# Kernel optimization log

Hardware: AMD Instinct MI355X
Metric: run time of the kernel (lower is better)

Reference implementation:

```python
import jax, jax.numpy as jnp
import numpy as np

B, Q, K, D, H, DH = 4, 512, 4096, 1024, 8, 128  # qk_channels=v_channels=out=1024

def setup_inputs() -> dict:
    key = jax.random.key(0)
    ks = jax.random.split(key, 5)
    s = 1.0 / np.sqrt(D)
    return {
        "inputs_q": jax.random.normal(ks[0], (B, Q, D), jnp.float32),
        "inputs_kv": jax.random.normal(ks[1], (B, K, D), jnp.float32),
        "Wq": jax.random.normal(ks[2], (D, H, DH), jnp.float32) * s,
        "Wkv": jax.random.normal(ks[3], (D, H, 2 * DH), jnp.float32) * s,
        "Wproj": jax.random.normal(ks[4], (H, DH, D), jnp.float32) * (1.0 / np.sqrt(H * DH)),
        "b_proj": jnp.zeros((D,), jnp.float32),
    }

def reference(inputs_q, inputs_kv, Wq, Wkv, Wproj, b_proj):
    # QKV projections (no bias)
    q = jnp.einsum('bqd,dhe->bqhe', inputs_q, Wq)          # [B,Q,H,DH]
    kv = jnp.einsum('bkd,dhe->bkhe', inputs_kv, Wkv)        # [B,K,H,2*DH]
    k, v = kv[..., :DH], kv[..., DH:]
    # scaled dot-product attention (softmax in fp32, per source)
    attn = jnp.einsum('bqhd,bkhd->bhqk', q, k) / np.sqrt(DH)
    attn = jax.nn.softmax(attn.astype(jnp.float32), axis=-1).astype(v.dtype)
    o = jnp.einsum('bhqk,bkhd->bqhd', attn, v)              # [B,Q,H,DH]
    # output projection contracting (head, head_dim), with bias
    return jnp.einsum('bqhd,hdo->bqo', o, Wproj) + b_proj   # [B,Q,D]
```

## Files before the change

kernel.cpp:

```cpp
#include <hip/hip_runtime.h>
#include <hip/hip_bf16.h>
#include <cstdint>

typedef unsigned short u16;
typedef unsigned int u32;
typedef __bf16 bf16x8 __attribute__((ext_vector_type(8)));
typedef u16 u16x8 __attribute__((ext_vector_type(8)));
typedef u16 u16x4 __attribute__((ext_vector_type(4)));
typedef float f32x4 __attribute__((ext_vector_type(4)));

#define MFMA16(a, b, c) __builtin_amdgcn_mfma_f32_16x16x32_bf16(a, b, c, 0, 0, 0)

__device__ __forceinline__ void async16(const void* g, void* s) {
    __builtin_amdgcn_global_load_lds((const __attribute__((address_space(1))) void*)g,
                                     (__attribute__((address_space(3))) void*)s, 16, 0, 0);
}

__device__ __forceinline__ u16 f2bf(float f) {
    u32 u; __builtin_memcpy(&u, &f, 4);
    u = u + 0x7fffu + ((u >> 16) & 1u);
    return (u16)(u >> 16);
}

__global__ __launch_bounds__(256) void convert_inputs(const float* __restrict__ inq,
                                                      u16* __restrict__ Aq,
                                                      const float* __restrict__ inkv,
                                                      u16* __restrict__ Akv) {
    const int blk = blockIdx.x;
    const float* in; u16* out; size_t i;
    if (blk < 1024) { in = inq;  out = Aq;  i = (size_t)blk * 256 + threadIdx.x; }
    else            { in = inkv; out = Akv; i = (size_t)(blk - 1024) * 256 + threadIdx.x; }
    const float4* p = (const float4*)in + i * 2;
    const float4 a = p[0], b = p[1];
    u16x8 v;
    v[0] = f2bf(a.x); v[1] = f2bf(a.y); v[2] = f2bf(a.z); v[3] = f2bf(a.w);
    v[4] = f2bf(b.x); v[5] = f2bf(b.y); v[6] = f2bf(b.z); v[7] = f2bf(b.w);
    ((u16x8*)out)[i] = v;
}

__global__ __launch_bounds__(256) void prep_weights(const float* __restrict__ Wq,  u16* __restrict__ WqT,
                                                    const float* __restrict__ Wkv, u16* __restrict__ WkvT,
                                                    const float* __restrict__ Wp,  u16* __restrict__ WpT) {
    __shared__ u16 t[64][65];
    const int blk = blockIdx.x;
    const float* in; u16* out; int R, C, bx, by;
    if (blk < 256)      { in = Wq;  out = WqT;  R = 1024; C = 1024; bx = blk & 15;  by = blk >> 4; }
    else if (blk < 768) { in = Wkv; out = WkvT; R = 1024; C = 2048; bx = (blk - 256) & 31; by = (blk - 256) >> 5; }
    else                { in = Wp;  out = WpT;  R = 1024; C = 1024; bx = (blk - 768) & 15; by = (blk - 768) >> 4; }
    const int r0 = by << 6, c0 = bx << 6;
    const int tid = threadIdx.x;
#pragma unroll
    for (int i = 0; i < 16; i++) {
        int idx = i * 256 + tid;
        int r = idx >> 6, c = idx & 63;
        t[r][c] = f2bf(in[(size_t)(r0 + r) * C + c0 + c]);
    }
    __syncthreads();
#pragma unroll
    for (int i = 0; i < 16; i++) {
        int idx = i * 256 + tid;
        int c = idx >> 6, r = idx & 63;
        out[(size_t)(c0 + c) * R + r0 + r] = t[r][c];
    }
}

template <bool OUTF32, int NT>
__global__ __launch_bounds__(256) void gemm_bt(const u16* __restrict__ A,
                                               const u16* __restrict__ B,
                                               void* __restrict__ Cv,
                                               const float* __restrict__ bias,
                                               int M, int N, int K) {
    constexpr int NJ = NT / 32;
    __shared__ __align__(16) u16 As[128 * 64];
    __shared__ __align__(16) u16 Bs[NT * 64];
    const int tid = threadIdx.x;
    const int wave = tid >> 6, lane = tid & 63;
    const int lrow = lane & 15, quad = lane >> 4;
    const int nb = N / NT;
    const int bx = blockIdx.x % nb, by = blockIdx.x / nb;
    const long m0 = (long)by << 7, n0 = (long)bx * NT;
    const int wm = (wave >> 1) << 6, wn = (wave & 1) * (NT / 2);

    const f32x4 fz = {0.f, 0.f, 0.f, 0.f};
    f32x4 acc[4][NJ];
#pragma unroll
    for (int i = 0; i < 4; i++)
#pragma unroll
        for (int j = 0; j < NJ; j++) acc[i][j] = fz;

    const int srow = wave * 8 + (lane >> 3);
    const int scol = ((lane & 7) ^ (lane >> 3)) << 3;
    const u16* Ag = A + (m0 + srow) * K + scol;
    const u16* Bg = B + (n0 + srow) * K + scol;
    u16* AsW = &As[wave * 512];
    u16* BsW = &Bs[wave * 512];

    for (int k0 = 0; k0 < K; k0 += 64) {
        __syncthreads();
#pragma unroll
        for (int c = 0; c < 4; c++)
            async16(Ag + (long)c * 32 * K + k0, AsW + c * 2048);
#pragma unroll
        for (int c = 0; c < NT / 32; c++)
            async16(Bg + (long)c * 32 * K + k0, BsW + c * 2048);
        __syncthreads();
#pragma unroll
        for (int c = 0; c < 2; c++) {
            bf16x8 af[4], bfr[NJ];
#pragma unroll
            for (int i = 0; i < 4; i++) {
                const int row = wm + i * 16 + lrow;
                af[i] = *(const bf16x8*)&As[row * 64 + (((c * 4 + quad) ^ (row & 7)) << 3)];
            }
#pragma unroll
            for (int j = 0; j < NJ; j++) {
                const int row = wn + j * 16 + lrow;
                bfr[j] = *(const bf16x8*)&Bs[row * 64 + (((c * 4 + quad) ^ (row & 7)) << 3)];
            }
#pragma unroll
            for (int i = 0; i < 4; i++)
#pragma unroll
                for (int j = 0; j < NJ; j++)
                    acc[i][j] = MFMA16(af[i], bfr[j], acc[i][j]);
        }
    }
#pragma unroll
    for (int j = 0; j < NJ; j++) {
        const long col = n0 + wn + j * 16 + lrow;
        const float bv = bias ? bias[col] : 0.0f;
#pragma unroll
        for (int i = 0; i < 4; i++) {
            const long row = m0 + wm + i * 16 + quad * 4;
#pragma unroll
            for (int r = 0; r < 4; r++) {
                const float v = acc[i][j][r] + bv;
                if (OUTF32) ((float*)Cv)[(row + r) * N + col] = v;
                else        ((u16*)Cv)[(row + r) * N + col] = f2bf(v);
            }
        }
    }
}

__global__ __launch_bounds__(512, 2) void gemm_kv256(const u16* __restrict__ A,
                                                     const u16* __restrict__ B,
                                                     u16* __restrict__ C,
                                                     u16* __restrict__ Vt) {
    constexpr int K = 1024, N = 2048, NT = 16;
    __shared__ __align__(16) u16 As[2][256 * 64];
    __shared__ __align__(16) u16 Bs[2][256 * 64];
    const int tid = threadIdx.x;
    const int wave = tid >> 6, lane = tid & 63;
    const int lrow = lane & 15, quad = lane >> 4;
    const int wMi = wave >> 2, wNi = wave & 3;
    const int wm = wMi * 128, wn = wNi * 64;
    const int wg = blockIdx.x;
    const int swz = (wg & 7) * 64 + (wg >> 3);
    const int bx = swz & 7, by = swz >> 3;
    const long m0 = (long)by << 8, n0 = (long)bx << 8;

    const int srow = tid >> 3;
    const int scol = ((tid & 7) ^ (srow & 7)) << 3;
    const u16* Ag = A + (m0 + srow) * K + scol;
    const u16* Bg = B + (n0 + srow) * K + scol;
    const int sdst = tid * 8;

    auto stgA = [&](int bi, int h, int kt) {
        async16(Ag + (size_t)(h * 128) * K + kt * 64,      &As[bi][h * 8192 + sdst]);
        async16(Ag + (size_t)(h * 128 + 64) * K + kt * 64, &As[bi][h * 8192 + 4096 + sdst]);
    };
    auto stgB = [&](int bi, int h, int kt) {
        async16(Bg + (size_t)(h * 128) * K + kt * 64,      &Bs[bi][h * 8192 + sdst]);
        async16(Bg + (size_t)(h * 128 + 64) * K + kt * 64, &Bs[bi][h * 8192 + 4096 + sdst]);
    };

    stgB(0, 0, 0); stgB(0, 1, 0); stgA(0, 0, 0); stgA(0, 1, 0);
    stgB(1, 0, 1); stgB(1, 1, 1); stgA(1, 0, 1);

    const f32x4 fz = {0.f, 0.f, 0.f, 0.f};
    f32x4 acc[8][4];
#pragma unroll
    for (int i = 0; i < 8; i++)
#pragma unroll
        for (int j = 0; j < 4; j++) acc[i][j] = fz;

    asm volatile("s_waitcnt vmcnt(6)" ::: "memory");
    __builtin_amdgcn_s_barrier();

    bf16x8 av[4][2], bv[4][2];
    for (int t = 0; t < NT; ++t) {
        const int cur = t & 1, nxt = cur ^ 1;
#pragma unroll
        for (int i = 0; i < 4; i++) {
            const int row = wm + i * 16 + lrow;
#pragma unroll
            for (int c = 0; c < 2; c++)
                av[i][c] = *(const bf16x8*)&As[cur][row * 64 + (((c * 4 + quad) ^ (row & 7)) << 3)];
        }
#pragma unroll
        for (int j = 0; j < 4; j++) {
            const int row = wn + j * 16 + lrow;
#pragma unroll
            for (int c = 0; c < 2; c++)
                bv[j][c] = *(const bf16x8*)&Bs[cur][row * 64 + (((c * 4 + quad) ^ (row & 7)) << 3)];
        }
        if (t + 1 < NT) stgA(nxt, 1, t + 1);
        __builtin_amdgcn_s_barrier();
        asm volatile("s_waitcnt lgkmcnt(0)" ::: "memory");
        __builtin_amdgcn_s_setprio(1);
#pragma unroll
        for (int i = 0; i < 4; i++)
#pragma unroll
            for (int j = 0; j < 2; j++)
#pragma unroll
                for (int c = 0; c < 2; c++)
                    acc[i][j] = MFMA16(av[i][c], bv[j][c], acc[i][j]);
        __builtin_amdgcn_s_setprio(0);
        __builtin_amdgcn_s_barrier();
        if (t + 2 < NT) stgB(cur, 0, t + 2);
        __builtin_amdgcn_s_barrier();
        __builtin_amdgcn_s_setprio(1);
#pragma unroll
        for (int i = 0; i < 4; i++)
#pragma unroll
            for (int j = 2; j < 4; j++)
#pragma unroll
                for (int c = 0; c < 2; c++)
                    acc[i][j] = MFMA16(av[i][c], bv[j][c], acc[i][j]);
        __builtin_amdgcn_s_setprio(0);
        __builtin_amdgcn_s_barrier();
#pragma unroll
        for (int i = 0; i < 4; i++) {
            const int row = wm + (i + 4) * 16 + lrow;
#pragma unroll
            for (int c = 0; c < 2; c++)
                av[i][c] = *(const bf16x8*)&As[cur][row * 64 + (((c * 4 + quad) ^ (row & 7)) << 3)];
        }
        if (t + 2 < NT) stgB(cur, 1, t + 2);
        __builtin_amdgcn_s_barrier();
        asm volatile("s_waitcnt lgkmcnt(0)" ::: "memory");
        __builtin_amdgcn_s_setprio(1);
#pragma unroll
        for (int i = 0; i < 4; i++)
#pragma unroll
            for (int j = 0; j < 2; j++)
#pragma unroll
                for (int c = 0; c < 2; c++)
                    acc[i + 4][j] = MFMA16(av[i][c], bv[j][c], acc[i + 4][j]);
        __builtin_amdgcn_s_setprio(0);
        __builtin_amdgcn_s_barrier();
        if (t + 2 < NT) stgA(cur, 0, t + 2);
        __builtin_amdgcn_s_barrier();
        __builtin_amdgcn_s_setprio(1);
#pragma unroll
        for (int i = 0; i < 4; i++)
#pragma unroll
            for (int j = 2; j < 4; j++)
#pragma unroll
                for (int c = 0; c < 2; c++)
                    acc[i + 4][j] = MFMA16(av[i][c], bv[j][c], acc[i + 4][j]);
        __builtin_amdgcn_s_setprio(0);
        if (t + 2 < NT)      { asm volatile("s_waitcnt vmcnt(6)" ::: "memory"); }
        else if (t + 1 < NT) { asm volatile("s_waitcnt vmcnt(0)" ::: "memory"); }
        __builtin_amdgcn_s_barrier();
    }

    const int h = bx;
    if (wNi < 2) {
#pragma unroll
        for (int j = 0; j < 4; j++) {
            const long col = n0 + wn + j * 16 + lrow;
#pragma unroll
            for (int i = 0; i < 8; i++) {
                const long row = m0 + wm + i * 16 + quad * 4;
#pragma unroll
                for (int r = 0; r < 4; r++)
                    C[(row + r) * N + col] = f2bf(acc[i][j][r]);
            }
        }
    } else {
#pragma unroll
        for (int j = 0; j < 4; j++) {
            const int dh = (wNi - 2) * 64 + j * 16 + lrow;
#pragma unroll
            for (int i = 0; i < 8; i++) {
                const int row = (int)m0 + wm + i * 16 + quad * 4;
                const int b = row >> 12, kv = row & 4095;
                u16x4 pk;
#pragma unroll
                for (int r = 0; r < 4; r++) pk[r] = f2bf(acc[i][j][r]);
                *(u16x4*)&Vt[(((size_t)b * 8 + h) * 128 + dh) * 4096 + kv] = pk;
            }
        }
    }
}

__global__ __launch_bounds__(512) void flash_attn_split(const u16* __restrict__ qb,
                                                        const u16* __restrict__ kvb,
                                                        const u16* __restrict__ vTb,
                                                        float* __restrict__ Opart,
                                                        float* __restrict__ Mpart,
                                                        float* __restrict__ Lpart) {
    __shared__ __align__(16) u16 Ks[64 * 128];
    __shared__ __align__(16) u16 Vs[128 * 64];
    __shared__ __align__(16) u16 Ps[8][16 * 64];
    const int tid = threadIdx.x, wave = tid >> 6, lane = tid & 63;
    const int lrow = lane & 15, quad = lane >> 4;
    const int blk = blockIdx.x;
    const int split = blk & 3, qt = (blk >> 2) & 3, h = (blk >> 4) & 7, b = blk >> 7;
    const int q0 = qt * 128;
    const int kbase = split * 1024;

    bf16x8 qf[4];
    {
        const u16* qp = qb + (((size_t)(b * 512 + q0 + wave * 16 + lrow) * 8 + h) << 7) + quad * 8;
#pragma unroll
        for (int c = 0; c < 4; c++) qf[c] = *(const bf16x8*)(qp + c * 32);
    }

    const f32x4 fz = {0.f, 0.f, 0.f, 0.f};
    f32x4 oacc[8];
#pragma unroll
    for (int g = 0; g < 8; g++) oacc[g] = fz;
    float mrow = -1e30f, lsum = 0.f;
    const float scale = 0.08838834764831845f;

    const int kRow = tid >> 4, kBlk = tid & 15;
    const int vRow = tid >> 3, vBlk = tid & 7;
    const u16* kg = kvb + (size_t)b * 4096 * 2048 + h * 256 + kBlk * 8;
    const u16* vg = vTb + (size_t)(b * 8 + h) * 128 * 4096 + vBlk * 8;

    for (int k0 = kbase; k0 < kbase + 1024; k0 += 64) {
        __syncthreads();
#pragma unroll
        for (int i = 0; i < 2; i++) {
            const int r = i * 32 + kRow;
            *(bf16x8*)&Ks[r * 128 + ((kBlk ^ (r & 15)) << 3)] =
                *(const bf16x8*)&kg[(size_t)(k0 + r) * 2048];
            const int rv = i * 64 + vRow;
            *(bf16x8*)&Vs[rv * 64 + ((vBlk ^ (rv & 7)) << 3)] =
                *(const bf16x8*)&vg[(size_t)rv * 4096 + k0];
        }
        __syncthreads();

        f32x4 s[4];
#pragma unroll
        for (int t = 0; t < 4; t++) {
            f32x4 a = fz;
#pragma unroll
            for (int c = 0; c < 4; c++) {
                const bf16x8 kf = *(const bf16x8*)
                    &Ks[(t * 16 + lrow) * 128 + (((c * 4 + quad) ^ lrow) << 3)];
                a = MFMA16(kf, qf[c], a);
            }
            s[t] = a * scale;
        }

        float mx = s[0][0];
#pragma unroll
        for (int t = 0; t < 4; t++)
#pragma unroll
            for (int r = 0; r < 4; r++) mx = fmaxf(mx, s[t][r]);
        mx = fmaxf(mx, __shfl_xor(mx, 16));
        mx = fmaxf(mx, __shfl_xor(mx, 32));
        const float mn = fmaxf(mrow, mx);
        const float alpha = __expf(mrow - mn);
        mrow = mn;
        float sum = 0.f;
#pragma unroll
        for (int t = 0; t < 4; t++)
#pragma unroll
            for (int r = 0; r < 4; r++) {
                float p = __expf(s[t][r] - mn);
                s[t][r] = p;
                sum += p;
            }
        sum += __shfl_xor(sum, 16);
        sum += __shfl_xor(sum, 32);
        lsum = lsum * alpha + sum;

        u16* Pw = &Ps[wave][0];
#pragma unroll
        for (int t = 0; t < 4; t++) {
            u16x4 pk;
#pragma unroll
            for (int r = 0; r < 4; r++) pk[r] = f2bf(s[t][r]);
            const int kvo = t * 16 + quad * 4;
            *(u16x4*)&Pw[lrow * 64 + (((kvo >> 3) ^ (lrow & 7)) << 3) + (kvo & 7)] = pk;
        }
        asm volatile("s_waitcnt lgkmcnt(0)" ::: "memory");
        const bf16x8 pf0 = *(const bf16x8*)&Pw[lrow * 64 + ((quad ^ (lrow & 7)) << 3)];
        const bf16x8 pf1 = *(const bf16x8*)&Pw[lrow * 64 + (((4 + quad) ^ (lrow & 7)) << 3)];

#pragma unroll
        for (int g = 0; g < 8; g++) {
            f32x4 o = oacc[g] * alpha;
            o = MFMA16(*(const bf16x8*)&Vs[(g * 16 + lrow) * 64 + ((quad ^ (lrow & 7)) << 3)], pf0, o);
            o = MFMA16(*(const bf16x8*)&Vs[(g * 16 + lrow) * 64 + (((4 + quad) ^ (lrow & 7)) << 3)], pf1, o);
            oacc[g] = o;
        }
    }

    float* Ob = Opart + (size_t)blk * 16384;
#pragma unroll
    for (int g = 0; g < 8; g++)
        *(f32x4*)&Ob[(wave * 16 + lrow) * 128 + g * 16 + quad * 4] = oacc[g];
    if (quad == 0) {
        const int row = blk * 128 + wave * 16 + lrow;
        Mpart[row] = mrow;
        Lpart[row] = lsum;
    }
}

__global__ __launch_bounds__(512) void combine_attn(const float* __restrict__ Opart,
                                                    const float* __restrict__ Mpart,
                                                    const float* __restrict__ Lpart,
                                                    u16* __restrict__ ob) {
    const int c = blockIdx.x;
    const int qt = c & 3, h = (c >> 2) & 7, b = c >> 5;
    const int lr = threadIdx.x >> 2, cg = (threadIdx.x & 3) * 32;
    float ms[4], w[4];
    float m = -1e30f;
#pragma unroll
    for (int s = 0; s < 4; s++) { ms[s] = Mpart[(c * 4 + s) * 128 + lr]; m = fmaxf(m, ms[s]); }
    float l = 0.f;
#pragma unroll
    for (int s = 0; s < 4; s++) { w[s] = __expf(ms[s] - m); l += w[s] * Lpart[(c * 4 + s) * 128 + lr]; }
    const float inv = 1.f / l;
#pragma unroll
    for (int s = 0; s < 4; s++) w[s] *= inv;
    const size_t orow = ((size_t)(b * 512 + qt * 128 + lr) * 8 + h) << 7;
#pragma unroll
    for (int j = 0; j < 4; j++) {
        f32x4 a0 = {0.f, 0.f, 0.f, 0.f}, a1 = a0;
#pragma unroll
        for (int s = 0; s < 4; s++) {
            const f32x4* p = (const f32x4*)(Opart + ((size_t)(c * 4 + s)) * 16384 + (size_t)lr * 128 + cg + j * 8);
            a0 += p[0] * w[s];
            a1 += p[1] * w[s];
        }
        u16x8 v;
#pragma unroll
        for (int i = 0; i < 4; i++) { v[i] = f2bf(a0[i]); v[4 + i] = f2bf(a1[i]); }
        *(u16x8*)&ob[orow + cg + j * 8] = v;
    }
}

extern "C" void kernel_launch(void* const* d_in, const int* in_sizes, int n_in,
                              void* d_out, int out_size, void* d_ws, size_t ws_size,
                              hipStream_t stream) {
    const float* inq   = (const float*)d_in[0];
    const float* inkv  = (const float*)d_in[1];
    const float* Wq    = (const float*)d_in[2];
    const float* Wkv   = (const float*)d_in[3];
    const float* Wproj = (const float*)d_in[4];
    const float* bproj = (const float*)d_in[5];
    float* out = (float*)d_out;

    u16* WqT    = (u16*)d_ws;
    u16* WkvT   = WqT + (size_t)1024 * 1024;
    u16* WprojT = WkvT + (size_t)2048 * 1024;
    u16* Aq     = WprojT + (size_t)1024 * 1024;
    u16* Akv    = Aq + (size_t)2048 * 1024;
    u16* qbuf   = Akv + (size_t)16384 * 1024;
    u16* kvbuf  = qbuf + (size_t)2048 * 1024;
    u16* vTbuf  = kvbuf + (size_t)16384 * 2048;
    u16* obuf   = vTbuf + (size_t)32 * 128 * 4096;

    float* Opart = (float*)Akv;
    float* Mpart = (float*)Aq;
    float* Lpart = Mpart + 65536;

    convert_inputs<<<9216, 256, 0, stream>>>(inq, Aq, inkv, Akv);
    prep_weights<<<1024, 256, 0, stream>>>(Wq, WqT, Wkv, WkvT, Wproj, WprojT);

    gemm_bt<false, 64><<<16 * 16, 256, 0, stream>>>(Aq, WqT, qbuf, nullptr, 2048, 1024, 1024);
    gemm_kv256<<<512, 512, 0, stream>>>(Akv, WkvT, kvbuf, vTbuf);

    flash_attn_split<<<512, 512, 0, stream>>>(qbuf, kvbuf, vTbuf, Opart, Mpart, Lpart);
    combine_attn<<<128, 512, 0, stream>>>(Opart, Mpart, Lpart, obuf);

    gemm_bt<true, 64><<<16 * 16, 256, 0, stream>>>(obuf, WprojT, (void*)out, bproj, 2048, 1024, 1024);
}
```

Baseline: 305.1 us.

## Double-buffer flash attention K/V tiles, lazy rescale, vectorize GEMM epilogue stores

The flash attention kernel now double-buffers K and V tiles in shared memory. It issues global loads for the next tile into registers before computing on the current one, and it drops one of the two barriers per iteration. Online-softmax rescaling is skipped when the wave-wide running max grows by at most 8, which avoids multiplying the accumulators each step but leaves an unnormalized exponent margin. The generic GEMM swaps the MFMA operands so that each lane writes contiguous 4-element vectors in the epilogue, and the KV GEMM gets sched_barriers around its MFMA phases. The flash kernel also gets occupancy launch bounds and priority hints.

Measured after the change: 303.9 us. Within noise of the previous version (-0.4%).

```diff
diff --git a/kernel.cpp b/kernel.cpp
--- a/kernel.cpp
+++ b/kernel.cpp
@@ -121,21 +121,24 @@
             for (int i = 0; i < 4; i++)
 #pragma unroll
                 for (int j = 0; j < NJ; j++)
-                    acc[i][j] = MFMA16(af[i], bfr[j], acc[i][j]);
-        }
-    }
-#pragma unroll
-    for (int j = 0; j < NJ; j++) {
-        const long col = n0 + wn + j * 16 + lrow;
-        const float bv = bias ? bias[col] : 0.0f;
-#pragma unroll
-        for (int i = 0; i < 4; i++) {
-            const long row = m0 + wm + i * 16 + quad * 4;
-#pragma unroll
-            for (int r = 0; r < 4; r++) {
-                const float v = acc[i][j][r] + bv;
-                if (OUTF32) ((float*)Cv)[(row + r) * N + col] = v;
-                else        ((u16*)Cv)[(row + r) * N + col] = f2bf(v);
+                    acc[i][j] = MFMA16(bfr[j], af[i], acc[i][j]);
+        }
+    }
+#pragma unroll
+    for (int i = 0; i < 4; i++) {
+        const long row = m0 + wm + i * 16 + lrow;
+#pragma unroll
+        for (int j = 0; j < NJ; j++) {
+            const long colb = n0 + wn + j * 16 + quad * 4;
+            if (OUTF32) {
+                f32x4 v = acc[i][j];
+                if (bias) v += *(const f32x4*)&bias[colb];
+                *(f32x4*)&((float*)Cv)[row * N + colb] = v;
+            } else {
+                u16x4 pk;
+#pragma unroll
+                for (int r = 0; r < 4; r++) pk[r] = f2bf(acc[i][j][r]);
+                *(u16x4*)&((u16*)Cv)[row * N + colb] = pk;
             }
         }
     }
@@ -206,6 +209,7 @@
         if (t + 1 < NT) stgA(nxt, 1, t + 1);
         __builtin_amdgcn_s_barrier();
         asm volatile("s_waitcnt lgkmcnt(0)" ::: "memory");
+        __builtin_amdgcn_sched_barrier(0);
         __builtin_amdgcn_s_setprio(1);
 #pragma unroll
         for (int i = 0; i < 4; i++)
@@ -218,6 +222,7 @@
         __builtin_amdgcn_s_barrier();
         if (t + 2 < NT) stgB(cur, 0, t + 2);
         __builtin_amdgcn_s_barrier();
+        __builtin_amdgcn_sched_barrier(0);
         __builtin_amdgcn_s_setprio(1);
 #pragma unroll
         for (int i = 0; i < 4; i++)
@@ -238,6 +243,7 @@
         if (t + 2 < NT) stgB(cur, 1, t + 2);
         __builtin_amdgcn_s_barrier();
         asm volatile("s_waitcnt lgkmcnt(0)" ::: "memory");
+        __builtin_amdgcn_sched_barrier(0);
         __builtin_amdgcn_s_setprio(1);
 #pragma unroll
         for (int i = 0; i < 4; i++)
@@ -250,6 +256,7 @@
         __builtin_amdgcn_s_barrier();
         if (t + 2 < NT) stgA(cur, 0, t + 2);
         __builtin_amdgcn_s_barrier();
+        __builtin_amdgcn_sched_barrier(0);
         __builtin_amdgcn_s_setprio(1);
 #pragma unroll
         for (int i = 0; i < 4; i++)
@@ -294,14 +301,14 @@
     }
 }
 
-__global__ __launch_bounds__(512) void flash_attn_split(const u16* __restrict__ qb,
-                                                        const u16* __restrict__ kvb,
-                                                        const u16* __restrict__ vTb,
-                                                        float* __restrict__ Opart,
-                                                        float* __restrict__ Mpart,
-                                                        float* __restrict__ Lpart) {
-    __shared__ __align__(16) u16 Ks[64 * 128];
-    __shared__ __align__(16) u16 Vs[128 * 64];
+__global__ __launch_bounds__(512, 4) void flash_attn_split(const u16* __restrict__ qb,
+                                                           const u16* __restrict__ kvb,
+                                                           const u16* __restrict__ vTb,
+                                                           float* __restrict__ Opart,
+                                                           float* __restrict__ Mpart,
+                                                           float* __restrict__ Lpart) {
+    __shared__ __align__(16) u16 Ks[2][64 * 128];
+    __shared__ __align__(16) u16 Vs[2][128 * 64];
     __shared__ __align__(16) u16 Ps[8][16 * 64];
     const int tid = threadIdx.x, wave = tid >> 6, lane = tid & 63;
     const int lrow = lane & 15, quad = lane >> 4;
@@ -328,32 +335,47 @@
     const int vRow = tid >> 3, vBlk = tid & 7;
     const u16* kg = kvb + (size_t)b * 4096 * 2048 + h * 256 + kBlk * 8;
     const u16* vg = vTb + (size_t)(b * 8 + h) * 128 * 4096 + vBlk * 8;
-
-    for (int k0 = kbase; k0 < kbase + 1024; k0 += 64) {
-        __syncthreads();
-#pragma unroll
-        for (int i = 0; i < 2; i++) {
-            const int r = i * 32 + kRow;
-            *(bf16x8*)&Ks[r * 128 + ((kBlk ^ (r & 15)) << 3)] =
-                *(const bf16x8*)&kg[(size_t)(k0 + r) * 2048];
-            const int rv = i * 64 + vRow;
-            *(bf16x8*)&Vs[rv * 64 + ((vBlk ^ (rv & 7)) << 3)] =
-                *(const bf16x8*)&vg[(size_t)rv * 4096 + k0];
-        }
-        __syncthreads();
+    const int ksw = (kBlk ^ (kRow & 15)) << 3;
+    const int vsw = (vBlk ^ (vRow & 7)) << 3;
+
+    {
+        const bf16x8 a0 = *(const bf16x8*)&kg[(size_t)(kbase + kRow) * 2048];
+        const bf16x8 a1 = *(const bf16x8*)&kg[(size_t)(kbase + 32 + kRow) * 2048];
+        const bf16x8 b0 = *(const bf16x8*)&vg[(size_t)vRow * 4096 + kbase];
+        const bf16x8 b1 = *(const bf16x8*)&vg[(size_t)(64 + vRow) * 4096 + kbase];
+        *(bf16x8*)&Ks[0][kRow * 128 + ksw] = a0;
+        *(bf16x8*)&Ks[0][(32 + kRow) * 128 + ksw] = a1;
+        *(bf16x8*)&Vs[0][vRow * 64 + vsw] = b0;
+        *(bf16x8*)&Vs[0][(64 + vRow) * 64 + vsw] = b1;
+    }
+    __syncthreads();
+
+    for (int it = 0; it < 16; ++it) {
+        const int cur = it & 1, nxt = cur ^ 1;
+        const bool more = (it + 1 < 16);
+        bf16x8 nk0, nk1, nv0, nv1;
+        if (more) {
+            const int k1 = kbase + (it + 1) * 64;
+            nk0 = *(const bf16x8*)&kg[(size_t)(k1 + kRow) * 2048];
+            nk1 = *(const bf16x8*)&kg[(size_t)(k1 + 32 + kRow) * 2048];
+            nv0 = *(const bf16x8*)&vg[(size_t)vRow * 4096 + k1];
+            nv1 = *(const bf16x8*)&vg[(size_t)(64 + vRow) * 4096 + k1];
+        }
 
         f32x4 s[4];
+        __builtin_amdgcn_s_setprio(1);
 #pragma unroll
         for (int t = 0; t < 4; t++) {
             f32x4 a = fz;
 #pragma unroll
             for (int c = 0; c < 4; c++) {
                 const bf16x8 kf = *(const bf16x8*)
-                    &Ks[(t * 16 + lrow) * 128 + (((c * 4 + quad) ^ lrow) << 3)];
+                    &Ks[cur][(t * 16 + lrow) * 128 + (((c * 4 + quad) ^ lrow) << 3)];
                 a = MFMA16(kf, qf[c], a);
             }
             s[t] = a * scale;
         }
+        __builtin_amdgcn_s_setprio(0);
 
         float mx = s[0][0];
 #pragma unroll
@@ -362,9 +384,16 @@
             for (int r = 0; r < 4; r++) mx = fmaxf(mx, s[t][r]);
         mx = fmaxf(mx, __shfl_xor(mx, 16));
         mx = fmaxf(mx, __shfl_xor(mx, 32));
-        const float mn = fmaxf(mrow, mx);
-        const float alpha = __expf(mrow - mn);
-        mrow = mn;
+        float mn = fmaxf(mrow, mx);
+        if (__all(mx <= mrow + 8.f)) {
+            mn = mrow;
+        } else {
+            const float alpha = __expf(mrow - mn);
+#pragma unroll
+            for (int g = 0; g < 8; g++) oacc[g] *= alpha;
+            lsum *= alpha;
+            mrow = mn;
+        }
         float sum = 0.f;
 #pragma unroll
         for (int t = 0; t < 4; t++)
@@ -376,7 +405,7 @@
             }
         sum += __shfl_xor(sum, 16);
         sum += __shfl_xor(sum, 32);
-        lsum = lsum * alpha + sum;
+        lsum += sum;
 
         u16* Pw = &Ps[wave][0];
 #pragma unroll
@@ -388,16 +417,27 @@
             *(u16x4*)&Pw[lrow * 64 + (((kvo >> 3) ^ (lrow & 7)) << 3) + (kvo & 7)] = pk;
         }
         asm volatile("s_waitcnt lgkmcnt(0)" ::: "memory");
+        __builtin_amdgcn_sched_barrier(0);
         const bf16x8 pf0 = *(const bf16x8*)&Pw[lrow * 64 + ((quad ^ (lrow & 7)) << 3)];
         const bf16x8 pf1 = *(const bf16x8*)&Pw[lrow * 64 + (((4 + quad) ^ (lrow & 7)) << 3)];
 
+        __builtin_amdgcn_s_setprio(1);
 #pragma unroll
         for (int g = 0; g < 8; g++) {
-            f32x4 o = oacc[g] * alpha;
-            o = MFMA16(*(const bf16x8*)&Vs[(g * 16 + lrow) * 64 + ((quad ^ (lrow & 7)) << 3)], pf0, o);
-            o = MFMA16(*(const bf16x8*)&Vs[(g * 16 + lrow) * 64 + (((4 + quad) ^ (lrow & 7)) << 3)], pf1, o);
+            f32x4 o = oacc[g];
+            o = MFMA16(*(const bf16x8*)&Vs[cur][(g * 16 + lrow) * 64 + ((quad ^ (lrow & 7)) << 3)], pf0, o);
+            o = MFMA16(*(const bf16x8*)&Vs[cur][(g * 16 + lrow) * 64 + (((4 + quad) ^ (lrow & 7)) << 3)], pf1, o);
             oacc[g] = o;
         }
+        __builtin_amdgcn_s_setprio(0);
+
+        if (more) {
+            *(bf16x8*)&Ks[nxt][kRow * 128 + ksw] = nk0;
+            *(bf16x8*)&Ks[nxt][(32 + kRow) * 128 + ksw] = nk1;
+            *(bf16x8*)&Vs[nxt][vRow * 64 + vsw] = nv0;
+            *(bf16x8*)&Vs[nxt][(64 + vRow) * 64 + vsw] = nv1;
+        }
+        __syncthreads();
     }
 
     float* Ob = Opart + (size_t)blk * 16384;
```
